# Optimization experiments

Measured on AMD Instinct MI355X. Metric: run time of the kernel, lower is better.

The kernel has to match this reference:

```python
import jax, jax.numpy as jnp
import numpy as np

B = 16384          # batch_size
NF = 50            # n_fields
K = 16             # embedding_dim
V = 1_000_000      # input_dim (vocab)
H = 400            # fc hidden
NNZ = B * NF


def _xavier(key, shape):
    fan_in, fan_out = shape
    lim = (6.0 / (fan_in + fan_out)) ** 0.5
    return jax.random.uniform(key, shape, minval=-lim, maxval=lim, dtype=jnp.float32)


def setup_inputs() -> dict:
    key = jax.random.key(0)
    ks = jax.random.split(key, 12)
    feats = jax.random.randint(ks[0], (NNZ,), 0, V)
    # n_fields contiguous features per sample (required by view(batch_size,-1))
    index = jnp.repeat(jnp.arange(B), NF)
    values = jax.random.uniform(ks[1], (NNZ,), dtype=jnp.float32)
    bias = jnp.zeros((1, 1), jnp.float32)
    weights = _xavier(ks[2], (V, 1))
    embedding = _xavier(ks[3], (V, K))
    d = NF * K  # 800
    W0 = _xavier(ks[4], (d, H))
    b0 = jax.random.normal(ks[5], (1, 1), jnp.float32)
    W1 = _xavier(ks[6], (H, H))
    b1 = jax.random.normal(ks[7], (1, 1), jnp.float32)
    W2 = _xavier(ks[8], (H, 1))
    b2 = jax.random.normal(ks[9], (1, 1), jnp.float32)
    return dict(index=index, feats=feats, values=values, bias=bias,
                weights=weights, embedding=embedding,
                W0=W0, b0=b0, W1=W1, b1=b1, W2=W2, b2=b2, batch_size=B)


def reference(index, feats, values, bias, weights, embedding,
              W0, b0, W1, b1, W2, b2, batch_size):
    # gather (F.embedding)
    w = weights[feats, 0]              # [nnz]
    emb = embedding[feats]             # [nnz, K]

    # first order: segment-sum of w*v, plus bias ([B] + [1,1] -> [1,B], as in torch)
    first = jax.ops.segment_sum(w * values, index, num_segments=batch_size) + bias

    # second order: FM pooling trick, fused over all K dims in one segment reduce
    ev = emb * values[:, None]                                        # [nnz, K]
    s1 = jax.ops.segment_sum(ev, index, num_segments=batch_size)      # [B, K]
    s2 = jax.ops.segment_sum(ev * ev, index, num_segments=batch_size) # [B, K]
    second = 0.5 * jnp.sum(s1 * s1 - s2, axis=1)                      # [B]

    # higher order MLP (relu on every layer, scalar biases)
    x = emb.reshape(batch_size, -1)    # [B, NF*K]
    x = jax.nn.relu(x @ W0 + b0)
    x = jax.nn.relu(x @ W1 + b1)
    x = jax.nn.relu(x @ W2 + b2)       # [B, 1]
    higher = x.reshape(-1)             # [B]

    return jax.nn.sigmoid(first + second + higher)  # [1, B]
```

## Files before the change

### kernel.cpp

```cpp
#include <hip/hip_runtime.h>
#include <hip/hip_bf16.h>


#define BATCH 16384
#define NFLD  50
#define EK    16
#define DDIM  800
#define HDIM  400
#define HPAD  416
#define NPAD  512

typedef __attribute__((ext_vector_type(8))) __bf16 bf16x8;
typedef __attribute__((ext_vector_type(4))) float  f32x4;

typedef const __attribute__((address_space(1))) unsigned int* gas_u32p;
typedef __attribute__((address_space(3))) unsigned int*       las_u32p;

__device__ __forceinline__ void gld_lds16(const void* g, void* l) {
    __builtin_amdgcn_global_load_lds((gas_u32p)g, (las_u32p)l, 16, 0, 0);
}

__global__ __launch_bounds__(256) void transpose_pad_kernel(
    const float* __restrict__ W0, const float* __restrict__ W1,
    __hip_bfloat16* __restrict__ W0t, __hip_bfloat16* __restrict__ W1t)
{
    const int which = blockIdx.z;
    if (which == 1 && blockIdx.x >= HPAD / 32) return;
    const float* src = which ? W1 : W0;
    __hip_bfloat16* dst = which ? W1t : W0t;
    const int srcK = which ? HDIM : DDIM;
    const int srcN = HDIM;
    const int dstCols = which ? HPAD : DDIM;

    __shared__ float tile[32][33];
    const int tx = threadIdx.x & 31, ty = threadIdx.x >> 5;
    const int k0 = blockIdx.x * 32, n0 = blockIdx.y * 32;
#pragma unroll
    for (int r = 0; r < 4; ++r) {
        int k = k0 + ty + r * 8;
        int n = n0 + tx;
        float v = (k < srcK && n < srcN) ? src[(long)k * srcN + n] : 0.f;
        tile[ty + r * 8][tx] = v;
    }
    __syncthreads();
#pragma unroll
    for (int r = 0; r < 4; ++r) {
        int n = n0 + ty + r * 8;
        int k = k0 + tx;
        dst[(long)n * dstCols + k] = __float2bfloat16(tile[tx][ty + r * 8]);
    }
}

__global__ __launch_bounds__(256) void gather_fm_kernel(
    const int* __restrict__ feats, const float* __restrict__ values,
    const float* __restrict__ biasp, const float* __restrict__ weights,
    const float* __restrict__ embedding,
    float* __restrict__ fs, __hip_bfloat16* __restrict__ x)
{
    const int wave = threadIdx.x >> 6;
    const int lane = threadIdx.x & 63;
    const int s    = blockIdx.x * 4 + wave;
    const int r    = lane >> 2, c = lane & 3;
    const long base = (long)s * NFLD;

    int   f = 0; float v = 0.f, wsum = 0.f;
    if (lane < NFLD) {
        f = feats[base + lane];
        v = values[base + lane];
        wsum = weights[f] * v;
    }

    int   fj[4]; float vj[4];
#pragma unroll
    for (int p = 0; p < 4; ++p) {
        const int j = p * 16 + r;
        if (p < 3 || r < 2) { fj[p] = __shfl(f, j); vj[p] = __shfl(v, j); }
    }
    float4 e[4];
#pragma unroll
    for (int p = 0; p < 4; ++p)
        if (p < 3 || r < 2)
            e[p] = *(const float4*)(embedding + (long)fj[p] * EK + c * 4);

    f32x4 s1 = {0.f, 0.f, 0.f, 0.f}, s2 = {0.f, 0.f, 0.f, 0.f};
#pragma unroll
    for (int p = 0; p < 4; ++p) {
        const int j = p * 16 + r;
        if (p < 3 || r < 2) {
            f32x4 ef = {e[p].x, e[p].y, e[p].z, e[p].w};
            f32x4 ev = ef * vj[p];
            s1 += ev;
            s2 += ev * ev;
            __hip_bfloat16 pk[4] = {
                __float2bfloat16(e[p].x), __float2bfloat16(e[p].y),
                __float2bfloat16(e[p].z), __float2bfloat16(e[p].w)};
            *(uint2*)&x[(long)s * DDIM + j * EK + c * 4] = *(uint2*)pk;
        }
    }
#pragma unroll
    for (int m = 4; m <= 32; m <<= 1) {
        s1.x += __shfl_xor(s1.x, m); s1.y += __shfl_xor(s1.y, m);
        s1.z += __shfl_xor(s1.z, m); s1.w += __shfl_xor(s1.w, m);
        s2.x += __shfl_xor(s2.x, m); s2.y += __shfl_xor(s2.y, m);
        s2.z += __shfl_xor(s2.z, m); s2.w += __shfl_xor(s2.w, m);
    }
    float t = (s1.x * s1.x - s2.x) + (s1.y * s1.y - s2.y)
            + (s1.z * s1.z - s2.z) + (s1.w * s1.w - s2.w);
    t += __shfl_xor(t, 1); t += __shfl_xor(t, 2);
    wsum += __shfl_xor(wsum, 1);  wsum += __shfl_xor(wsum, 2);
    wsum += __shfl_xor(wsum, 4);  wsum += __shfl_xor(wsum, 8);
    wsum += __shfl_xor(wsum, 16); wsum += __shfl_xor(wsum, 32);
    if (lane == 0) fs[s] = wsum + 0.5f * t + biasp[0];
}

template <int KDIM, int MODE, int LDC>
__global__ __launch_bounds__(256) void gemm_relu_kernel(
    const __hip_bfloat16* __restrict__ A,
    const __hip_bfloat16* __restrict__ Bt,
    const float* __restrict__ biasp,
    const float* __restrict__ W2,
    void* __restrict__ C)
{
    constexpr int KT = KDIM / 32;
    __shared__ __align__(16) __hip_bfloat16 sA[128 * 32];
    __shared__ __align__(16) __hip_bfloat16 sB[128 * 32];

    const int tid  = threadIdx.x;
    const int wave = tid >> 6, lane = tid & 63;
    const int l16  = lane & 15, quad = lane >> 4;
    const int waveM = wave & 1, waveN = wave >> 1;
    const int m0 = blockIdx.y * 128;
    const int n0 = blockIdx.x * 128;

    f32x4 acc[4][4] = {};

    const long ar0 = (long)(m0 + wave * 16 + (lane >> 2)) * KDIM;
    const long ar1 = ar0 + (long)64 * KDIM;
    const long br0 = (long)(n0 + wave * 16 + (lane >> 2)) * KDIM;
    const long br1 = br0 + (long)64 * KDIM;
    const int  ac  = (lane & 3) * 8;
    __hip_bfloat16* ldsA0 = sA + wave * 512 + lane * 8;
    __hip_bfloat16* ldsA1 = sA + 2048 + wave * 512 + lane * 8;
    __hip_bfloat16* ldsB0 = sB + wave * 512 + lane * 8;
    __hip_bfloat16* ldsB1 = sB + 2048 + wave * 512 + lane * 8;

    for (int kt = 0; kt < KT; ++kt) {
        const int k0 = kt * 32;
        gld_lds16(A  + ar0 + k0 + ac, ldsA0);
        gld_lds16(A  + ar1 + k0 + ac, ldsA1);
        gld_lds16(Bt + br0 + k0 + ac, ldsB0);
        gld_lds16(Bt + br1 + k0 + ac, ldsB1);
        __syncthreads();

        bf16x8 af[4], bfr[4];
#pragma unroll
        for (int i = 0; i < 4; ++i)
            af[i] = *(const bf16x8*)&sA[(waveM * 64 + i * 16 + l16) * 32 + quad * 8];
#pragma unroll
        for (int j = 0; j < 4; ++j)
            bfr[j] = *(const bf16x8*)&sB[(waveN * 64 + j * 16 + l16) * 32 + quad * 8];
#pragma unroll
        for (int i = 0; i < 4; ++i)
#pragma unroll
            for (int j = 0; j < 4; ++j)
                acc[i][j] = __builtin_amdgcn_mfma_f32_16x16x32_bf16(
                    af[i], bfr[j], acc[i][j], 0, 0, 0);
        __syncthreads();
    }

    const float bias = biasp[0];
    if constexpr (MODE == 0) {
#pragma unroll
        for (int i = 0; i < 4; ++i) {
            const int row = m0 + waveM * 64 + i * 16 + quad * 4;
#pragma unroll
            for (int j = 0; j < 4; ++j) {
                const int col = n0 + waveN * 64 + j * 16 + l16;
#pragma unroll
                for (int r = 0; r < 4; ++r) {
                    float v = acc[i][j][r] + bias;
                    v = v > 0.f ? v : 0.f;
                    __hip_bfloat16* Cp = (__hip_bfloat16*)C;
                    if (col < HDIM)
                        Cp[(long)(row + r) * LDC + col] = __float2bfloat16(v);
                    else if (col < LDC)
                        Cp[(long)(row + r) * LDC + col] = __float2bfloat16(0.f);
                }
            }
        }
    } else {
        float w2v[4];
#pragma unroll
        for (int j = 0; j < 4; ++j) {
            int col = n0 + waveN * 64 + j * 16 + l16;
            w2v[j] = (col < HDIM) ? W2[col] : 0.f;
        }
        const int slot = blockIdx.x * 2 + waveN;
#pragma unroll
        for (int i = 0; i < 4; ++i) {
#pragma unroll
            for (int r = 0; r < 4; ++r) {
                float p = 0.f;
#pragma unroll
                for (int j = 0; j < 4; ++j) {
                    float v = acc[i][j][r] + bias;
                    v = v > 0.f ? v : 0.f;
                    p += v * w2v[j];
                }
                p += __shfl_xor(p, 1); p += __shfl_xor(p, 2);
                p += __shfl_xor(p, 4); p += __shfl_xor(p, 8);
                if (l16 == 0) {
                    int row = m0 + waveM * 64 + i * 16 + quad * 4 + r;
                    ((float*)C)[(long)row * 8 + slot] = p;
                }
            }
        }
    }
}

__global__ __launch_bounds__(256) void final_kernel(
    const float* __restrict__ partial, const float* __restrict__ b2p,
    const float* __restrict__ fs, float* __restrict__ out)
{
    const int s = blockIdx.x * 256 + threadIdx.x;
    const float4 p0 = *(const float4*)(partial + (long)s * 8);
    const float4 p1 = *(const float4*)(partial + (long)s * 8 + 4);
    float sum = (p0.x + p0.y) + (p0.z + p0.w) + (p1.x + p1.y) + (p1.z + p1.w);
    float h = sum + b2p[0];
    h = h > 0.f ? h : 0.f;
    float z = fs[s] + h;
    out[s] = 1.f / (1.f + __expf(-z));
}

extern "C" void kernel_launch(void* const* d_in, const int* in_sizes, int n_in,
                              void* d_out, int out_size, void* d_ws, size_t ws_size,
                              hipStream_t stream)
{
    const int*   feats     = (const int*)d_in[1];
    const float* values    = (const float*)d_in[2];
    const float* bias      = (const float*)d_in[3];
    const float* weights   = (const float*)d_in[4];
    const float* embedding = (const float*)d_in[5];
    const float* W0 = (const float*)d_in[6];
    const float* b0 = (const float*)d_in[7];
    const float* W1 = (const float*)d_in[8];
    const float* b1 = (const float*)d_in[9];
    const float* W2 = (const float*)d_in[10];
    const float* b2 = (const float*)d_in[11];

    char* ws = (char*)d_ws;
    size_t off = 0;
    auto alloc = [&](size_t bytes) {
        void* p = ws + off;
        off += (bytes + 255) & ~(size_t)255;
        return p;
    };
    float*          fs   = (float*)alloc((size_t)BATCH * 4);
    __hip_bfloat16* x    = (__hip_bfloat16*)alloc((size_t)BATCH * DDIM * 2);
    __hip_bfloat16* h0   = (__hip_bfloat16*)alloc((size_t)BATCH * HPAD * 2);
    float*          part = (float*)alloc((size_t)BATCH * 8 * 4);
    __hip_bfloat16* W0t  = (__hip_bfloat16*)alloc((size_t)NPAD * DDIM * 2);
    __hip_bfloat16* W1t  = (__hip_bfloat16*)alloc((size_t)NPAD * HPAD * 2);
    (void)ws_size; (void)in_sizes; (void)n_in; (void)out_size;

    transpose_pad_kernel<<<dim3(DDIM / 32, NPAD / 32, 2), 256, 0, stream>>>(
        W0, W1, W0t, W1t);
    gather_fm_kernel<<<dim3(BATCH / 4), 256, 0, stream>>>(
        feats, values, bias, weights, embedding, fs, x);
    gemm_relu_kernel<DDIM, 0, HPAD>
        <<<dim3(NPAD / 128, BATCH / 128), 256, 0, stream>>>(
        x, W0t, b0, nullptr, (void*)h0);
    gemm_relu_kernel<HPAD, 1, 8>
        <<<dim3(NPAD / 128, BATCH / 128), 256, 0, stream>>>(
        h0, W1t, b1, W2, (void*)part);
    final_kernel<<<dim3(BATCH / 256), 256, 0, stream>>>(
        part, b2, fs, (float*)d_out);
}
```

Baseline: 187.9 us.

## Process two K tiles per barrier and stage GEMM output through LDS

```diff
diff --git a/kernel.cpp b/kernel.cpp
--- a/kernel.cpp
+++ b/kernel.cpp
@@ -6,8 +6,9 @@
 #define NFLD  50
 #define EK    16
 #define DDIM  800
+#define DPAD  832
 #define HDIM  400
-#define HPAD  416
+#define HPAD  448
 #define NPAD  512
 
 typedef __attribute__((ext_vector_type(8))) __bf16 bf16x8;
@@ -30,7 +31,7 @@
     __hip_bfloat16* dst = which ? W1t : W0t;
     const int srcK = which ? HDIM : DDIM;
     const int srcN = HDIM;
-    const int dstCols = which ? HPAD : DDIM;
+    const int dstCols = which ? HPAD : DPAD;
 
     __shared__ float tile[32][33];
     const int tx = threadIdx.x & 31, ty = threadIdx.x >> 5;
@@ -94,9 +95,11 @@
             __hip_bfloat16 pk[4] = {
                 __float2bfloat16(e[p].x), __float2bfloat16(e[p].y),
                 __float2bfloat16(e[p].z), __float2bfloat16(e[p].w)};
-            *(uint2*)&x[(long)s * DDIM + j * EK + c * 4] = *(uint2*)pk;
-        }
-    }
+            *(uint2*)&x[(long)s * DPAD + j * EK + c * 4] = *(uint2*)pk;
+        }
+    }
+    if (lane < 16) *(unsigned int*)&x[(long)s * DPAD + DDIM + lane * 2] = 0u;
+
 #pragma unroll
     for (int m = 4; m <= 32; m <<= 1) {
         s1.x += __shfl_xor(s1.x, m); s1.y += __shfl_xor(s1.y, m);
@@ -113,6 +116,7 @@
     if (lane == 0) fs[s] = wsum + 0.5f * t + biasp[0];
 }
 
+#define OSTRIDE 136
 template <int KDIM, int MODE, int LDC>
 __global__ __launch_bounds__(256) void gemm_relu_kernel(
     const __hip_bfloat16* __restrict__ A,
@@ -122,8 +126,10 @@
     void* __restrict__ C)
 {
     constexpr int KT = KDIM / 32;
-    __shared__ __align__(16) __hip_bfloat16 sA[128 * 32];
-    __shared__ __align__(16) __hip_bfloat16 sB[128 * 32];
+    __shared__ __align__(16) char lds[128 * OSTRIDE * 2];
+    __hip_bfloat16* sA = (__hip_bfloat16*)lds;
+    __hip_bfloat16* sB = sA + 2 * 4096;
+    __hip_bfloat16* sO = (__hip_bfloat16*)lds;
 
     const int tid  = threadIdx.x;
     const int wave = tid >> 6, lane = tid & 63;
@@ -144,27 +150,32 @@
     __hip_bfloat16* ldsB0 = sB + wave * 512 + lane * 8;
     __hip_bfloat16* ldsB1 = sB + 2048 + wave * 512 + lane * 8;
 
-    for (int kt = 0; kt < KT; ++kt) {
-        const int k0 = kt * 32;
-        gld_lds16(A  + ar0 + k0 + ac, ldsA0);
-        gld_lds16(A  + ar1 + k0 + ac, ldsA1);
-        gld_lds16(Bt + br0 + k0 + ac, ldsB0);
-        gld_lds16(Bt + br1 + k0 + ac, ldsB1);
+    for (int kt = 0; kt < KT; kt += 2) {
+#pragma unroll
+        for (int h = 0; h < 2; ++h) {
+            const int k0 = (kt + h) * 32;
+            gld_lds16(A  + ar0 + k0 + ac, ldsA0 + h * 4096);
+            gld_lds16(A  + ar1 + k0 + ac, ldsA1 + h * 4096);
+            gld_lds16(Bt + br0 + k0 + ac, ldsB0 + h * 4096);
+            gld_lds16(Bt + br1 + k0 + ac, ldsB1 + h * 4096);
+        }
         __syncthreads();
-
-        bf16x8 af[4], bfr[4];
-#pragma unroll
-        for (int i = 0; i < 4; ++i)
-            af[i] = *(const bf16x8*)&sA[(waveM * 64 + i * 16 + l16) * 32 + quad * 8];
-#pragma unroll
-        for (int j = 0; j < 4; ++j)
-            bfr[j] = *(const bf16x8*)&sB[(waveN * 64 + j * 16 + l16) * 32 + quad * 8];
-#pragma unroll
-        for (int i = 0; i < 4; ++i)
+#pragma unroll
+        for (int h = 0; h < 2; ++h) {
+            bf16x8 af[4], bfr[4];
+#pragma unroll
+            for (int i = 0; i < 4; ++i)
+                af[i] = *(const bf16x8*)&sA[h * 4096 + (waveM * 64 + i * 16 + l16) * 32 + quad * 8];
 #pragma unroll
             for (int j = 0; j < 4; ++j)
-                acc[i][j] = __builtin_amdgcn_mfma_f32_16x16x32_bf16(
-                    af[i], bfr[j], acc[i][j], 0, 0, 0);
+                bfr[j] = *(const bf16x8*)&sB[h * 4096 + (waveN * 64 + j * 16 + l16) * 32 + quad * 8];
+#pragma unroll
+            for (int i = 0; i < 4; ++i)
+#pragma unroll
+                for (int j = 0; j < 4; ++j)
+                    acc[i][j] = __builtin_amdgcn_mfma_f32_16x16x32_bf16(
+                        af[i], bfr[j], acc[i][j], 0, 0, 0);
+        }
         __syncthreads();
     }
 
@@ -172,21 +183,30 @@
     if constexpr (MODE == 0) {
 #pragma unroll
         for (int i = 0; i < 4; ++i) {
-            const int row = m0 + waveM * 64 + i * 16 + quad * 4;
+            const int rl = waveM * 64 + i * 16 + quad * 4;
 #pragma unroll
             for (int j = 0; j < 4; ++j) {
-                const int col = n0 + waveN * 64 + j * 16 + l16;
+                const int cl = waveN * 64 + j * 16 + l16;
+                const int gcol = n0 + cl;
 #pragma unroll
                 for (int r = 0; r < 4; ++r) {
                     float v = acc[i][j][r] + bias;
                     v = v > 0.f ? v : 0.f;
-                    __hip_bfloat16* Cp = (__hip_bfloat16*)C;
-                    if (col < HDIM)
-                        Cp[(long)(row + r) * LDC + col] = __float2bfloat16(v);
-                    else if (col < LDC)
-                        Cp[(long)(row + r) * LDC + col] = __float2bfloat16(0.f);
+                    if (gcol >= HDIM) v = 0.f;
+                    sO[(rl + r) * OSTRIDE + cl] = __float2bfloat16(v);
                 }
             }
+        }
+        __syncthreads();
+        __hip_bfloat16* Cp = (__hip_bfloat16*)C;
+#pragma unroll
+        for (int q = 0; q < 8; ++q) {
+            const int flat = tid + q * 256;
+            const int rl = flat >> 4, c16 = flat & 15;
+            const int gcol = n0 + c16 * 8;
+            if (gcol < LDC)
+                *(float4*)&Cp[(long)(m0 + rl) * LDC + gcol] =
+                    *(const float4*)&sO[rl * OSTRIDE + c16 * 8];
         }
     } else {
         float w2v[4];
@@ -256,18 +276,18 @@
         return p;
     };
     float*          fs   = (float*)alloc((size_t)BATCH * 4);
-    __hip_bfloat16* x    = (__hip_bfloat16*)alloc((size_t)BATCH * DDIM * 2);
+    __hip_bfloat16* x    = (__hip_bfloat16*)alloc((size_t)BATCH * DPAD * 2);
     __hip_bfloat16* h0   = (__hip_bfloat16*)alloc((size_t)BATCH * HPAD * 2);
     float*          part = (float*)alloc((size_t)BATCH * 8 * 4);
-    __hip_bfloat16* W0t  = (__hip_bfloat16*)alloc((size_t)NPAD * DDIM * 2);
+    __hip_bfloat16* W0t  = (__hip_bfloat16*)alloc((size_t)NPAD * DPAD * 2);
     __hip_bfloat16* W1t  = (__hip_bfloat16*)alloc((size_t)NPAD * HPAD * 2);
     (void)ws_size; (void)in_sizes; (void)n_in; (void)out_size;
 
-    transpose_pad_kernel<<<dim3(DDIM / 32, NPAD / 32, 2), 256, 0, stream>>>(
+    transpose_pad_kernel<<<dim3(DPAD / 32, NPAD / 32, 2), 256, 0, stream>>>(
         W0, W1, W0t, W1t);
     gather_fm_kernel<<<dim3(BATCH / 4), 256, 0, stream>>>(
         feats, values, bias, weights, embedding, fs, x);
-    gemm_relu_kernel<DDIM, 0, HPAD>
+    gemm_relu_kernel<DPAD, 0, HPAD>
         <<<dim3(NPAD / 128, BATCH / 128), 256, 0, stream>>>(
         x, W0t, b0, nullptr, (void*)h0);
     gemm_relu_kernel<HPAD, 1, 8>
```

Result: faster. 181.2 us (-3.6%).
